# Optimization experiments

Hardware: AMD Instinct MI355X
Metric: run time of the kernel (lower is better)

The kernel has to match this reference:

```python
import jax, jax.numpy as jnp
import numpy as np

DIM = 3072
NUM_HEADS = 24
HEAD_DIM = DIM // NUM_HEADS  # 128
SEQ = 2048
BATCH = 1


def rms_norm(x, scale):
    # compute in fp32 like the torch module
    xf = x.astype(jnp.float32)
    rrms = jax.lax.rsqrt(jnp.mean(xf * xf, axis=-1, keepdims=True) + 1e-6)
    return (xf * rrms).astype(x.dtype) * scale


def apply_rope(xq, xk, pe):
    # xq, xk: [B, H, L, D]; pe: [B, 1, L, D//2, 2, 2]
    shp = xq.shape
    xq_ = xq.reshape(*shp[:-1], -1, 1, 2).astype(jnp.float32)
    xk_ = xk.reshape(*shp[:-1], -1, 1, 2).astype(jnp.float32)
    xq_out = pe[..., 0] * xq_[..., 0] + pe[..., 1] * xq_[..., 1]
    xk_out = pe[..., 0] * xk_[..., 0] + pe[..., 1] * xk_[..., 1]
    return xq_out.reshape(shp).astype(xq.dtype), xk_out.reshape(shp).astype(xk.dtype)


def setup_inputs() -> dict:
    key = jax.random.key(0)
    ks = jax.random.split(key, 6)
    s = 1.0 / np.sqrt(DIM)
    return {
        "x": jax.random.normal(ks[0], (BATCH, SEQ, DIM), dtype=jnp.float32),
        "pe": jax.random.normal(ks[1], (BATCH, 1, SEQ, HEAD_DIM // 2, 2, 2), dtype=jnp.float32),
        "w_qkv": jax.random.normal(ks[2], (3 * DIM, DIM), dtype=jnp.float32) * s,
        "w_proj": jax.random.normal(ks[3], (DIM, DIM), dtype=jnp.float32) * s,
        "b_proj": jax.random.normal(ks[4], (DIM,), dtype=jnp.float32) * 0.01,
        "q_scale": jnp.ones((HEAD_DIM,), dtype=jnp.float32),
        "k_scale": jnp.ones((HEAD_DIM,), dtype=jnp.float32),
    }


def reference(x, pe, w_qkv, w_proj, b_proj, q_scale, k_scale):
    B, L, _ = x.shape
    # fused qkv projection (qkv_bias=False)
    qkv = jnp.einsum("bld,ed->ble", x, w_qkv)  # [B, L, 3*DIM]
    qkv = qkv.reshape(B, L, 3, NUM_HEADS, HEAD_DIM)
    qkv = jnp.transpose(qkv, (2, 0, 3, 1, 4))  # [3, B, H, L, D]
    q, k, v = qkv[0], qkv[1], qkv[2]
    # QKNorm (RMSNorm on head_dim)
    q = rms_norm(q, q_scale).astype(v.dtype)
    k = rms_norm(k, k_scale).astype(v.dtype)
    # rope
    q, k = apply_rope(q, k, pe)
    # scaled dot-product attention
    scale = 1.0 / np.sqrt(HEAD_DIM)
    scores = jnp.einsum("bhqd,bhkd->bhqk", q, k) * scale
    probs = jax.nn.softmax(scores, axis=-1)
    out = jnp.einsum("bhqk,bhkd->bhqd", probs, v)
    out = jnp.transpose(out, (0, 2, 1, 3)).reshape(B, L, DIM)  # merge heads
    # output projection
    return jnp.einsum("bld,ed->ble", out, w_proj) + b_proj
```

## Files before the change

kernel.cpp:

```cpp
#include <hip/hip_runtime.h>

typedef __bf16 bf16;
typedef __attribute__((ext_vector_type(8))) __bf16 bf16x8;
typedef __attribute__((ext_vector_type(4))) float f32x4;

typedef __attribute__((address_space(1))) void gvoid_t;
typedef __attribute__((address_space(3))) void lvoid_t;

#define LDS_LOAD16(gp, lp) \
    __builtin_amdgcn_global_load_lds((gvoid_t*)(gp), (lvoid_t*)(lp), 16, 0, 0)

__global__ __launch_bounds__(256)
void f32_to_bf16(const float* __restrict__ in, bf16* __restrict__ out, int n8)
{
    const int i = blockIdx.x * 256 + threadIdx.x;
    if (i >= n8) return;
    const float4 a = ((const float4*)in)[i * 2];
    const float4 b = ((const float4*)in)[i * 2 + 1];
    bf16x8 o;
    o[0] = (bf16)a.x; o[1] = (bf16)a.y; o[2] = (bf16)a.z; o[3] = (bf16)a.w;
    o[4] = (bf16)b.x; o[5] = (bf16)b.y; o[6] = (bf16)b.z; o[7] = (bf16)b.w;
    *(bf16x8*)(out + (size_t)i * 8) = o;
}

template <int BIAS, typename CT>
__global__ __launch_bounds__(256, 2)
void gemm_bt(const bf16* __restrict__ A, const bf16* __restrict__ B,
             const float* __restrict__ bias, CT* __restrict__ C,
             int K, int ldc)
{
    __shared__ bf16 sA[128 * 32];
    __shared__ bf16 sB[128 * 32];
    const int tid  = threadIdx.x;
    const int lane = tid & 63;
    const int wid  = tid >> 6;
    const int m0 = blockIdx.y * 128;
    const int n0 = blockIdx.x * 128;
    const int wm = (wid >> 1) * 64;
    const int wn = (wid & 1) * 64;
    const int l15   = lane & 15;
    const int quad8 = (lane >> 4) * 8;

    f32x4 acc[4][4] = {};

    for (int k0 = 0; k0 < K; k0 += 32) {
#pragma unroll
        for (int t = 0; t < 2; ++t) {
            const int e  = (t * 4 + wid) * 512;
            const int ge = e + lane * 8;
            const int r = ge >> 5, c = ge & 31;
            LDS_LOAD16(A + (size_t)(m0 + r) * K + k0 + c, sA + e);
            LDS_LOAD16(B + (size_t)(n0 + r) * K + k0 + c, sB + e);
        }
        __syncthreads();

        bf16x8 af[4], bfr[4];
#pragma unroll
        for (int i = 0; i < 4; ++i) {
            af[i]  = *(const bf16x8*)(sA + (wm + i * 16 + l15) * 32 + quad8);
            bfr[i] = *(const bf16x8*)(sB + (wn + i * 16 + l15) * 32 + quad8);
        }
#pragma unroll
        for (int i = 0; i < 4; ++i)
#pragma unroll
            for (int j = 0; j < 4; ++j)
                acc[i][j] = __builtin_amdgcn_mfma_f32_16x16x32_bf16(af[i], bfr[j], acc[i][j], 0, 0, 0);
        __syncthreads();
    }

    const int rowBase = m0 + wm + (lane >> 4) * 4;
    const int colBase = n0 + wn + l15;
#pragma unroll
    for (int j = 0; j < 4; ++j) {
        const int col = colBase + j * 16;
        const float bv = BIAS ? bias[col] : 0.0f;
#pragma unroll
        for (int i = 0; i < 4; ++i) {
            const int row = rowBase + i * 16;
#pragma unroll
            for (int r = 0; r < 4; ++r)
                C[(size_t)(row + r) * ldc + col] = (CT)(acc[i][j][r] + bv);
        }
    }
}

__global__ __launch_bounds__(256)
void qk_rope_rearrange(const bf16* __restrict__ qkv, const float* __restrict__ pe,
                       const float* __restrict__ qs, const float* __restrict__ ks,
                       bf16* __restrict__ Qh, bf16* __restrict__ Kh, bf16* __restrict__ Vt)
{
    const int lane = threadIdx.x & 63;
    const int wid  = threadIdx.x >> 6;
    const int idx  = blockIdx.x * 4 + wid;
    const int h = idx >> 11;
    const int l = idx & 2047;

    const size_t rowb = (size_t)l * 9216 + h * 128 + 2 * lane;
    const float q0 = (float)qkv[rowb];
    const float q1 = (float)qkv[rowb + 1];
    const float k0 = (float)qkv[rowb + 3072];
    const float k1 = (float)qkv[rowb + 3073];
    const bf16  v0 = qkv[rowb + 6144];
    const bf16  v1 = qkv[rowb + 6145];

    float ssq = q0 * q0 + q1 * q1;
    float ssk = k0 * k0 + k1 * k1;
#pragma unroll
    for (int off = 1; off < 64; off <<= 1) {
        ssq += __shfl_xor(ssq, off);
        ssk += __shfl_xor(ssk, off);
    }
    const float rq = rsqrtf(ssq * (1.0f / 128.0f) + 1e-6f);
    const float rk = rsqrtf(ssk * (1.0f / 128.0f) + 1e-6f);

    const float s0q = qs[2 * lane], s1q = qs[2 * lane + 1];
    const float s0k = ks[2 * lane], s1k = ks[2 * lane + 1];

    const float qn0 = (q0 * rq) * s0q;
    const float qn1 = (q1 * rq) * s1q;
    const float kn0 = (k0 * rk) * s0k;
    const float kn1 = (k1 * rk) * s1k;

    const float* pp = pe + ((size_t)l * 64 + lane) * 4;
    const float p00 = pp[0], p01 = pp[1];
    const float p10 = pp[2], p11 = pp[3];

    const bf16 qo0 = (bf16)(p00 * qn0 + p01 * qn1);
    const bf16 qo1 = (bf16)(p10 * qn0 + p11 * qn1);
    const bf16 ko0 = (bf16)(p00 * kn0 + p01 * kn1);
    const bf16 ko1 = (bf16)(p10 * kn0 + p11 * kn1);

    const size_t ob = ((size_t)h * 2048 + l) * 128 + 2 * lane;
    Qh[ob] = qo0; Qh[ob + 1] = qo1;
    Kh[ob] = ko0; Kh[ob + 1] = ko1;

    const size_t vb = ((size_t)h * 128 + 2 * lane) * 2048 + l;
    Vt[vb]        = v0;
    Vt[vb + 2048] = v1;
}

__global__ __launch_bounds__(256, 2)
void flash_attn(const bf16* __restrict__ Qh, const bf16* __restrict__ Kh,
                const bf16* __restrict__ Vt, bf16* __restrict__ AO)
{
    __shared__ bf16 sK[2 * 64 * 128];
    __shared__ bf16 sV[2 * 128 * 64];
    __shared__ bf16 sP[4 * 16 * 72];

    const int tid   = threadIdx.x;
    const int lane  = tid & 63;
    const int wid   = tid >> 6;
    const int h     = blockIdx.y;
    const int qw    = blockIdx.x * 64 + wid * 16;
    const int l15   = lane & 15;
    const int quad  = lane >> 4;
    const int quad8 = quad * 8;

    const bf16* Kbase = Kh + (size_t)h * 2048 * 128;
    const bf16* Vbase = Vt + (size_t)h * 128 * 2048;

    bf16x8 aq[4];
    {
        const bf16* qp = Qh + ((size_t)h * 2048 + qw + l15) * 128 + quad8;
#pragma unroll
        for (int ki = 0; ki < 4; ++ki) aq[ki] = *(const bf16x8*)(qp + ki * 32);
    }

    bf16x8 ones;
#pragma unroll
    for (int i = 0; i < 8; ++i) ones[i] = (bf16)1.0f;

    f32x4 o[8] = {};
    f32x4 lacc = {};

    bf16* sPw = sP + wid * (16 * 72);
    const int slotbase = wid * 64;

#define STAGE_K(kv, buf)                                                         \
    {                                                                            \
        bf16* kb = sK + (buf) * (64 * 128);                                      \
        _Pragma("unroll")                                                        \
        for (int t = 0; t < 4; ++t) {                                            \
            const int sb   = t * 256 + slotbase;                                 \
            const int slot = sb + lane;                                          \
            const int r    = slot >> 4;                                          \
            const int cg   = (slot & 15) ^ (r & 7);                              \
            LDS_LOAD16(Kbase + (size_t)((kv) + r) * 128 + cg * 8, kb + sb * 8);  \
        }                                                                        \
    }
#define STAGE_V(kv, buf)                                                         \
    {                                                                            \
        bf16* vb = sV + (buf) * (128 * 64);                                      \
        _Pragma("unroll")                                                        \
        for (int t = 0; t < 4; ++t) {                                            \
            const int sb   = t * 256 + slotbase;                                 \
            const int slot = sb + lane;                                          \
            const int r    = slot >> 3;                                          \
            const int cg   = (slot & 7) ^ (r & 7);                               \
            LDS_LOAD16(Vbase + (size_t)r * 2048 + (kv) + cg * 8, vb + sb * 8);   \
        }                                                                        \
    }

    STAGE_K(0, 0);
    STAGE_V(0, 0);

    for (int s = 0; s < 32; ++s) {
        __syncthreads();
        if (s < 31) {
            STAGE_K((s + 1) * 64, (s + 1) & 1);
            STAGE_V((s + 1) * 64, (s + 1) & 1);
        }

        const bf16* kb = sK + (s & 1) * (64 * 128);
        const bf16* vb = sV + (s & 1) * (128 * 64);

        f32x4 sc[4];
#pragma unroll
        for (int nt = 0; nt < 4; ++nt) {
            f32x4 t = {};
            const int row = nt * 16 + l15;
#pragma unroll
            for (int ki = 0; ki < 4; ++ki) {
                const int pcg = (4 * ki + quad) ^ (l15 & 7);
                bf16x8 bk = *(const bf16x8*)(kb + row * 128 + pcg * 8);
                t = __builtin_amdgcn_mfma_f32_16x16x32_bf16(aq[ki], bk, t, 0, 0, 0);
            }
            sc[nt] = t;
        }

#pragma unroll
        for (int r = 0; r < 4; ++r) {
            const float scl = 0.08838834764831845f;
            bf16* pw = sPw + (quad * 4 + r) * 72 + l15;
            pw[0]  = (bf16)__expf(sc[0][r] * scl);
            pw[16] = (bf16)__expf(sc[1][r] * scl);
            pw[32] = (bf16)__expf(sc[2][r] * scl);
            pw[48] = (bf16)__expf(sc[3][r] * scl);
        }

#pragma unroll
        for (int kk = 0; kk < 2; ++kk) {
            bf16x8 pa = *(const bf16x8*)(sPw + l15 * 72 + kk * 32 + quad8);
            lacc = __builtin_amdgcn_mfma_f32_16x16x32_bf16(pa, ones, lacc, 0, 0, 0);
#pragma unroll
            for (int dt = 0; dt < 8; ++dt) {
                const int row = dt * 16 + l15;
                const int pcg = (kk * 4 + quad) ^ (l15 & 7);
                bf16x8 bv = *(const bf16x8*)(vb + row * 64 + pcg * 8);
                o[dt] = __builtin_amdgcn_mfma_f32_16x16x32_bf16(pa, bv, o[dt], 0, 0, 0);
            }
        }
    }
#undef STAGE_K
#undef STAGE_V

#pragma unroll
    for (int r = 0; r < 4; ++r) {
        const float inv = 1.0f / lacc[r];
        const size_t row = qw + quad * 4 + r;
        bf16* op = AO + row * 3072 + h * 128 + l15;
#pragma unroll
        for (int dt = 0; dt < 8; ++dt) op[dt * 16] = (bf16)(o[dt][r] * inv);
    }
}

extern "C" void kernel_launch(void* const* d_in, const int* in_sizes, int n_in,
                              void* d_out, int out_size, void* d_ws, size_t ws_size,
                              hipStream_t stream)
{
    (void)in_sizes; (void)n_in; (void)out_size;

    const float* x      = (const float*)d_in[0];
    const float* pe     = (const float*)d_in[1];
    const float* w_qkv  = (const float*)d_in[2];
    const float* w_proj = (const float*)d_in[3];
    const float* b_proj = (const float*)d_in[4];
    const float* q_s    = (const float*)d_in[5];
    const float* k_s    = (const float*)d_in[6];
    float* out = (float*)d_out;

    const size_t NEED_BIG = ((size_t)6291456 + 28311552 + 18874368 + 6291456) * 2;

    if (ws_size >= NEED_BIG) {
        bf16* xb  = (bf16*)d_ws;
        bf16* wb  = xb + (size_t)6291456;
        bf16* qkv = wb + (size_t)28311552;
        bf16* Vt  = qkv + (size_t)18874368;
        bf16* Qh  = xb;
        bf16* Kh  = wb;
        bf16* wpb = qkv;
        bf16* AO  = qkv + (size_t)9437184;

        f32_to_bf16<<<dim3(3072),  256, 0, stream>>>(x,     xb, 786432);
        f32_to_bf16<<<dim3(13824), 256, 0, stream>>>(w_qkv, wb, 3538944);
        gemm_bt<0, bf16><<<dim3(72, 16), 256, 0, stream>>>(xb, wb, nullptr, qkv, 3072, 9216);
        qk_rope_rearrange<<<dim3(12288), 256, 0, stream>>>(qkv, pe, q_s, k_s, Qh, Kh, Vt);
        f32_to_bf16<<<dim3(4608), 256, 0, stream>>>(w_proj, wpb, 1179648);
        flash_attn<<<dim3(32, 24), 256, 0, stream>>>(Qh, Kh, Vt, AO);
        gemm_bt<1, float><<<dim3(24, 16), 256, 0, stream>>>(AO, wpb, b_proj, out, 3072, 3072);
    } else {
        bf16* xb  = (bf16*)d_ws;
        bf16* wb  = xb + (size_t)6291456;
        bf16* qkv = wb + (size_t)9437184;
        bf16* Vt  = qkv + (size_t)18874368;
        bf16* Qh  = xb;
        bf16* Kh  = wb;
        bf16* wpb = qkv;
        bf16* AO  = qkv + (size_t)9437184;

        f32_to_bf16<<<dim3(3072), 256, 0, stream>>>(x, xb, 786432);
        for (int c = 0; c < 3; ++c) {
            f32_to_bf16<<<dim3(4608), 256, 0, stream>>>(w_qkv + (size_t)c * 9437184, wb, 1179648);
            gemm_bt<0, bf16><<<dim3(24, 16), 256, 0, stream>>>(xb, wb, nullptr, qkv + c * 3072, 3072, 9216);
        }
        qk_rope_rearrange<<<dim3(12288), 256, 0, stream>>>(qkv, pe, q_s, k_s, Qh, Kh, Vt);
        f32_to_bf16<<<dim3(4608), 256, 0, stream>>>(w_proj, wpb, 1179648);
        flash_attn<<<dim3(32, 24), 256, 0, stream>>>(Qh, Kh, Vt, AO);
        gemm_bt<1, float><<<dim3(24, 16), 256, 0, stream>>>(AO, wpb, b_proj, out, 3072, 3072);
    }
}
```

Before: 598.0 us.

## Fuse fp32-to-bf16 weight conversion into GEMM B-tile loads and swizzle LDS

```diff
diff --git a/kernel.cpp b/kernel.cpp
--- a/kernel.cpp
+++ b/kernel.cpp
@@ -25,7 +25,7 @@
 
 template <int BIAS, typename CT>
 __global__ __launch_bounds__(256, 2)
-void gemm_bt(const bf16* __restrict__ A, const bf16* __restrict__ B,
+void gemm_bt(const bf16* __restrict__ A, const float* __restrict__ B,
              const float* __restrict__ bias, CT* __restrict__ C,
              int K, int ldc)
 {
@@ -39,26 +39,42 @@
     const int wm = (wid >> 1) * 64;
     const int wn = (wid & 1) * 64;
     const int l15   = lane & 15;
-    const int quad8 = (lane >> 4) * 8;
+    const int quad  = lane >> 4;
 
     f32x4 acc[4][4] = {};
 
     for (int k0 = 0; k0 < K; k0 += 32) {
 #pragma unroll
+        for (int u = 0; u < 2; ++u) {
+            const int slot = u * 256 + tid;
+            const int r  = slot >> 2;
+            const int pg = slot & 3;
+            const int gc = (pg ^ ((r >> 1) & 3)) * 8;
+            const float4 f0 = *(const float4*)(B + (size_t)(n0 + r) * K + k0 + gc);
+            const float4 f1 = *(const float4*)(B + (size_t)(n0 + r) * K + k0 + gc + 4);
+            bf16x8 v;
+            v[0] = (bf16)f0.x; v[1] = (bf16)f0.y; v[2] = (bf16)f0.z; v[3] = (bf16)f0.w;
+            v[4] = (bf16)f1.x; v[5] = (bf16)f1.y; v[6] = (bf16)f1.z; v[7] = (bf16)f1.w;
+            *(bf16x8*)(sB + slot * 8) = v;
+        }
+#pragma unroll
         for (int t = 0; t < 2; ++t) {
-            const int e  = (t * 4 + wid) * 512;
-            const int ge = e + lane * 8;
-            const int r = ge >> 5, c = ge & 31;
-            LDS_LOAD16(A + (size_t)(m0 + r) * K + k0 + c, sA + e);
-            LDS_LOAD16(B + (size_t)(n0 + r) * K + k0 + c, sB + e);
+            const int sb   = t * 256 + wid * 64;
+            const int slot = sb + lane;
+            const int r  = slot >> 2;
+            const int pg = slot & 3;
+            const int gc = (pg ^ ((r >> 1) & 3)) * 8;
+            LDS_LOAD16(A + (size_t)(m0 + r) * K + k0 + gc, sA + slot * 8);
         }
         __syncthreads();
 
         bf16x8 af[4], bfr[4];
 #pragma unroll
         for (int i = 0; i < 4; ++i) {
-            af[i]  = *(const bf16x8*)(sA + (wm + i * 16 + l15) * 32 + quad8);
-            bfr[i] = *(const bf16x8*)(sB + (wn + i * 16 + l15) * 32 + quad8);
+            const int ra = wm + i * 16 + l15;
+            const int rb = wn + i * 16 + l15;
+            af[i]  = *(const bf16x8*)(sA + ra * 32 + ((quad ^ ((ra >> 1) & 3)) * 8));
+            bfr[i] = *(const bf16x8*)(sB + rb * 32 + ((quad ^ ((rb >> 1) & 3)) * 8));
         }
 #pragma unroll
         for (int i = 0; i < 4; ++i)
@@ -68,7 +84,7 @@
         __syncthreads();
     }
 
-    const int rowBase = m0 + wm + (lane >> 4) * 4;
+    const int rowBase = m0 + wm + quad * 4;
     const int colBase = n0 + wn + l15;
 #pragma unroll
     for (int j = 0; j < 4; ++j) {
@@ -268,7 +284,7 @@
                               void* d_out, int out_size, void* d_ws, size_t ws_size,
                               hipStream_t stream)
 {
-    (void)in_sizes; (void)n_in; (void)out_size;
+    (void)in_sizes; (void)n_in; (void)out_size; (void)ws_size;
 
     const float* x      = (const float*)d_in[0];
     const float* pe     = (const float*)d_in[1];
@@ -279,43 +295,16 @@
     const float* k_s    = (const float*)d_in[6];
     float* out = (float*)d_out;
 
-    const size_t NEED_BIG = ((size_t)6291456 + 28311552 + 18874368 + 6291456) * 2;
-
-    if (ws_size >= NEED_BIG) {
-        bf16* xb  = (bf16*)d_ws;
-        bf16* wb  = xb + (size_t)6291456;
-        bf16* qkv = wb + (size_t)28311552;
-        bf16* Vt  = qkv + (size_t)18874368;
-        bf16* Qh  = xb;
-        bf16* Kh  = wb;
-        bf16* wpb = qkv;
-        bf16* AO  = qkv + (size_t)9437184;
-
-        f32_to_bf16<<<dim3(3072),  256, 0, stream>>>(x,     xb, 786432);
-        f32_to_bf16<<<dim3(13824), 256, 0, stream>>>(w_qkv, wb, 3538944);
-        gemm_bt<0, bf16><<<dim3(72, 16), 256, 0, stream>>>(xb, wb, nullptr, qkv, 3072, 9216);
-        qk_rope_rearrange<<<dim3(12288), 256, 0, stream>>>(qkv, pe, q_s, k_s, Qh, Kh, Vt);
-        f32_to_bf16<<<dim3(4608), 256, 0, stream>>>(w_proj, wpb, 1179648);
-        flash_attn<<<dim3(32, 24), 256, 0, stream>>>(Qh, Kh, Vt, AO);
-        gemm_bt<1, float><<<dim3(24, 16), 256, 0, stream>>>(AO, wpb, b_proj, out, 3072, 3072);
-    } else {
-        bf16* xb  = (bf16*)d_ws;
-        bf16* wb  = xb + (size_t)6291456;
-        bf16* qkv = wb + (size_t)9437184;
-        bf16* Vt  = qkv + (size_t)18874368;
-        bf16* Qh  = xb;
-        bf16* Kh  = wb;
-        bf16* wpb = qkv;
-        bf16* AO  = qkv + (size_t)9437184;
-
-        f32_to_bf16<<<dim3(3072), 256, 0, stream>>>(x, xb, 786432);
-        for (int c = 0; c < 3; ++c) {
-            f32_to_bf16<<<dim3(4608), 256, 0, stream>>>(w_qkv + (size_t)c * 9437184, wb, 1179648);
-            gemm_bt<0, bf16><<<dim3(24, 16), 256, 0, stream>>>(xb, wb, nullptr, qkv + c * 3072, 3072, 9216);
-        }
-        qk_rope_rearrange<<<dim3(12288), 256, 0, stream>>>(qkv, pe, q_s, k_s, Qh, Kh, Vt);
-        f32_to_bf16<<<dim3(4608), 256, 0, stream>>>(w_proj, wpb, 1179648);
-        flash_attn<<<dim3(32, 24), 256, 0, stream>>>(Qh, Kh, Vt, AO);
-        gemm_bt<1, float><<<dim3(24, 16), 256, 0, stream>>>(AO, wpb, b_proj, out, 3072, 3072);
-    }
-}
+    bf16* xb  = (bf16*)d_ws;
+    bf16* qkv = xb + (size_t)6291456;
+    bf16* Kh  = qkv + (size_t)18874368;
+    bf16* Vt  = Kh + (size_t)6291456;
+    bf16* Qh  = xb;
+    bf16* AO  = qkv;
+
+    f32_to_bf16<<<dim3(3072), 256, 0, stream>>>(x, xb, 786432);
+    gemm_bt<0, bf16><<<dim3(72, 16), 256, 0, stream>>>(xb, w_qkv, nullptr, qkv, 3072, 9216);
+    qk_rope_rearrange<<<dim3(12288), 256, 0, stream>>>(qkv, pe, q_s, k_s, Qh, Kh, Vt);
+    flash_attn<<<dim3(32, 24), 256, 0, stream>>>(Qh, Kh, Vt, AO);
+    gemm_bt<1, float><<<dim3(24, 16), 256, 0, stream>>>(AO, w_proj, b_proj, out, 3072, 3072);
+}
```

New measurement: 652.1 us. 1.09x slower.
